# Kernel optimization log

Measured on AMD Instinct MI355X. Metric: run time of the kernel, lower is better.

The kernel has to match this reference:

```python
import jax, jax.numpy as jnp
import numpy as np


def setup_inputs() -> dict:
    key = jax.random.key(0)
    k1, k2, k3 = jax.random.split(key, 3)
    B, S, H, L = 64, 512, 768, 9  # batch, seq_len, bert hidden, num_labels
    sequence_output = jax.random.normal(k1, (B, S, H), dtype=jnp.float32)
    valid_mask = jax.random.randint(k2, (B, S), 0, 2, dtype=jnp.int32)
    W = jax.random.normal(k3, (H, L), dtype=jnp.float32) * 0.02  # TruncatedNormal stddev ~ initializer_range
    b = jnp.zeros((L,), dtype=jnp.float32)
    return {"sequence_output": sequence_output, "valid_mask": valid_mask, "W": W, "b": b}


def reference(sequence_output, valid_mask, W, b):
    # Per-row stream compaction: tokens with valid_mask==1 are moved to the
    # front of their row (stable order); remaining slots stay zero.
    B, S, H = sequence_output.shape
    pos = jnp.cumsum(valid_mask, axis=1) - 1           # destination index for valid tokens
    safe = jnp.where(valid_mask == 1, pos, S)           # invalid tokens -> dump slot S
    batch = jnp.arange(B)[:, None]                      # [B,1]
    valid_output = (
        jnp.zeros((B, S + 1, H), dtype=sequence_output.dtype)
        .at[batch, safe]
        .set(sequence_output)
    )[:, :S]                                            # drop dump slot
    # dropout is identity at inference (training=False)
    logits = jax.nn.softmax(valid_output @ W + b, axis=-1)  # [B,S,L]
    return logits
```

## Files before the change

### kernel.cpp

```cpp
#include <hip/hip_runtime.h>

#define B_ 64
#define S_ 512
#define H_ 768
#define L_ 9
#define TPB 16
#define BPR (S_ / TPB)
#define NPASS 1

__device__ __forceinline__ void bias_softmax(const float* __restrict__ bias,
                                             float* cprob) {
    float m = -3.4e38f;
#pragma unroll
    for (int c = 0; c < L_; c++) { cprob[c] = bias[c]; m = fmaxf(m, cprob[c]); }
    float s = 0.0f;
#pragma unroll
    for (int c = 0; c < L_; c++) { cprob[c] = __expf(cprob[c] - m); s += cprob[c]; }
    const float inv = 1.0f / s;
#pragma unroll
    for (int c = 0; c < L_; c++) cprob[c] *= inv;
}

__global__ __launch_bounds__(256, 4) void ner_kernel(const float* __restrict__ seq,
                                                     const int* __restrict__ mask,
                                                     const float* __restrict__ W,
                                                     const float* __restrict__ bias,
                                                     float* __restrict__ out) {
    __shared__ float wt[L_ * 3 * 64 * 4];
    __shared__ float bsh[16];
    __shared__ int   srcrow[S_];
    __shared__ int   wsum[4];

    const int tid  = threadIdx.x;
    const int lane = tid & 63;
    const int w    = tid >> 6;
    const int row  = blockIdx.x & 63;
    const int sub  = blockIdx.x >> 6;

    const int e0 = 2 * tid;
    const int2 mv = *reinterpret_cast<const int2*>(mask + row * S_ + e0);
    const int v0 = (mv.x != 0);
    const int v1 = (mv.y != 0);
    const unsigned long long b0 = __ballot(v0);
    const unsigned long long b1 = __ballot(v1);
    const unsigned long long lt = (1ULL << lane) - 1ULL;
    const int pfx  = __popcll(b0 & lt) + __popcll(b1 & lt);
    const int wtot = __popcll(b0) + __popcll(b1);
    if (lane == 0) wsum[w] = wtot;
    __syncthreads();

    const int cnt = wsum[0] + wsum[1] + wsum[2] + wsum[3];

    if (sub * TPB >= cnt) {
        float cprob[L_];
        bias_softmax(bias, cprob);
        const int base = (row * S_ + sub * TPB) * L_;
        for (int idx = tid; idx < TPB * L_; idx += 256)
            out[base + idx] = cprob[idx % L_];
        return;
    }

    int woff = 0;
#pragma unroll
    for (int i = 0; i < 4; i++)
        if (i < w) woff += wsum[i];
    const int p0 = woff + pfx;
    if (v0) srcrow[p0] = e0;
    if (v1) srcrow[p0 + v0] = e0 + 1;

    for (int idx = tid; idx < H_ * L_; idx += 256) {
        float val = W[idx];
        int h  = idx / 9;
        int c  = idx - 9 * h;
        int j  = h >> 8;
        int r  = h & 255;
        int ln = r >> 2;
        int k  = r & 3;
        wt[((c * 3 + j) * 64 + ln) * 4 + k] = val;
    }
    if (tid < 16) bsh[tid] = (tid < L_) ? bias[tid] : 0.0f;
    __syncthreads();

    const int cls = ((lane & 1) << 3) | (((lane >> 1) & 1) << 2)
                  | (((lane >> 2) & 1) << 1) | ((lane >> 3) & 1);
    const float bb = bsh[cls];
    const int g = lane >> 4;

    const float4* wt4 = reinterpret_cast<const float4*>(wt);

    for (int pass = 0; pass < NPASS; pass++) {
        const int basep = sub * TPB + w * (4 * NPASS) + pass * 4;

        if (basep >= cnt) {
            float cprob[L_];
            bias_softmax(bias, cprob);
            if (lane < 36)
                out[((size_t)row * S_ + basep) * L_ + lane] = cprob[lane % L_];
            continue;
        }

        float x[4][12];
#pragma unroll
        for (int t = 0; t < 4; t++) {
            const int pp = basep + t;
            if (pp < cnt) {
                const int src = srcrow[pp];
                const float4* p4 = reinterpret_cast<const float4*>(
                    seq + ((size_t)row * S_ + src) * H_) + lane;
                float4 a0 = p4[0], a1 = p4[64], a2 = p4[128];
                x[t][0] = a0.x; x[t][1] = a0.y; x[t][2]  = a0.z; x[t][3]  = a0.w;
                x[t][4] = a1.x; x[t][5] = a1.y; x[t][6]  = a1.z; x[t][7]  = a1.w;
                x[t][8] = a2.x; x[t][9] = a2.y; x[t][10] = a2.z; x[t][11] = a2.w;
            } else {
#pragma unroll
                for (int k = 0; k < 12; k++) x[t][k] = 0.0f;
            }
        }

        float acc[4][L_];
#pragma unroll
        for (int t = 0; t < 4; t++)
#pragma unroll
            for (int c = 0; c < L_; c++) acc[t][c] = 0.0f;

#pragma unroll
        for (int c = 0; c < L_; c++) {
#pragma unroll
            for (int j4 = 0; j4 < 3; j4++) {
                float4 wv = wt4[(c * 3 + j4) * 64 + lane];
#pragma unroll
                for (int t = 0; t < 4; t++) {
                    acc[t][c] += x[t][j4 * 4 + 0] * wv.x + x[t][j4 * 4 + 1] * wv.y
                               + x[t][j4 * 4 + 2] * wv.z + x[t][j4 * 4 + 3] * wv.w;
                }
            }
        }

        float logit[4];
#pragma unroll
        for (int t = 0; t < 4; t++) {
            float v[16];
#pragma unroll
            for (int c = 0; c < L_; c++) v[c] = acc[t][c];
#pragma unroll
            for (int c = L_; c < 16; c++) v[c] = 0.0f;

            {
                const bool b = (lane & 1);
#pragma unroll
                for (int i = 0; i < 8; i++) {
                    float give = b ? v[i] : v[i + 8];
                    float got  = __shfl_xor(give, 1);
                    v[i] = (b ? v[i + 8] : v[i]) + got;
                }
            }
            {
                const bool b = ((lane >> 1) & 1);
#pragma unroll
                for (int i = 0; i < 4; i++) {
                    float give = b ? v[i] : v[i + 4];
                    float got  = __shfl_xor(give, 2);
                    v[i] = (b ? v[i + 4] : v[i]) + got;
                }
            }
            {
                const bool b = ((lane >> 2) & 1);
#pragma unroll
                for (int i = 0; i < 2; i++) {
                    float give = b ? v[i] : v[i + 2];
                    float got  = __shfl_xor(give, 4);
                    v[i] = (b ? v[i + 2] : v[i]) + got;
                }
            }
            {
                const bool b = ((lane >> 3) & 1);
                float give = b ? v[0] : v[1];
                float got  = __shfl_xor(give, 8);
                v[0] = (b ? v[1] : v[0]) + got;
            }
            v[0] += __shfl_xor(v[0], 16);
            v[0] += __shfl_xor(v[0], 32);
            logit[t] = v[0];
        }

        float lg = (g == 0) ? logit[0] : (g == 1) ? logit[1]
                 : (g == 2) ? logit[2] : logit[3];
        lg += bb;
        float lx = (cls < L_) ? lg : -1e30f;
        float m = lx;
        m = fmaxf(m, __shfl_xor(m, 1));
        m = fmaxf(m, __shfl_xor(m, 2));
        m = fmaxf(m, __shfl_xor(m, 4));
        m = fmaxf(m, __shfl_xor(m, 8));
        float e = (cls < L_) ? __expf(lx - m) : 0.0f;
        float ssum = e;
        ssum += __shfl_xor(ssum, 1);
        ssum += __shfl_xor(ssum, 2);
        ssum += __shfl_xor(ssum, 4);
        ssum += __shfl_xor(ssum, 8);
        if (cls < L_)
            out[((size_t)row * S_ + basep + g) * L_ + cls] = e / ssum;
    }
}

extern "C" void kernel_launch(void* const* d_in, const int* in_sizes, int n_in,
                              void* d_out, int out_size, void* d_ws, size_t ws_size,
                              hipStream_t stream) {
    const float* seq  = (const float*)d_in[0];
    const int*   mask = (const int*)d_in[1];
    const float* W    = (const float*)d_in[2];
    const float* bias = (const float*)d_in[3];
    float*       out  = (float*)d_out;

    ner_kernel<<<B_ * BPR, 256, 0, stream>>>(seq, mask, W, bias, out);
}
```

Baseline: 147.0 us.

## Compute per-wave compaction via ballot select and issue token loads before weight staging

Each wave now reads the whole mask row itself and builds per-64-lane ballot prefix counts in registers, dropping the shared srcrow/wsum arrays and the first block barrier. Source rows are found with a binary popcount select, and the activation gathers are issued before the weight transpose into LDS so global latency overlaps the staging. The launch-bounds occupancy hint is removed and the bias is read from global memory. In exchange, every wave does redundant mask loads and select arithmetic, and register pressure rises because x is held across the barrier.

```diff
diff --git a/kernel.cpp b/kernel.cpp
--- a/kernel.cpp
+++ b/kernel.cpp
@@ -6,7 +6,6 @@
 #define L_ 9
 #define TPB 16
 #define BPR (S_ / TPB)
-#define NPASS 1
 
 __device__ __forceinline__ void bias_softmax(const float* __restrict__ bias,
                                              float* cprob) {
@@ -21,35 +20,33 @@
     for (int c = 0; c < L_; c++) cprob[c] *= inv;
 }
 
-__global__ __launch_bounds__(256, 4) void ner_kernel(const float* __restrict__ seq,
-                                                     const int* __restrict__ mask,
-                                                     const float* __restrict__ W,
-                                                     const float* __restrict__ bias,
-                                                     float* __restrict__ out) {
+__global__ __launch_bounds__(256) void ner_kernel(const float* __restrict__ seq,
+                                                  const int* __restrict__ mask,
+                                                  const float* __restrict__ W,
+                                                  const float* __restrict__ bias,
+                                                  float* __restrict__ out) {
     __shared__ float wt[L_ * 3 * 64 * 4];
-    __shared__ float bsh[16];
-    __shared__ int   srcrow[S_];
-    __shared__ int   wsum[4];
 
     const int tid  = threadIdx.x;
     const int lane = tid & 63;
-    const int w    = tid >> 6;
+    const int w    = __builtin_amdgcn_readfirstlane(tid >> 6);
     const int row  = blockIdx.x & 63;
     const int sub  = blockIdx.x >> 6;
 
-    const int e0 = 2 * tid;
-    const int2 mv = *reinterpret_cast<const int2*>(mask + row * S_ + e0);
-    const int v0 = (mv.x != 0);
-    const int v1 = (mv.y != 0);
-    const unsigned long long b0 = __ballot(v0);
-    const unsigned long long b1 = __ballot(v1);
-    const unsigned long long lt = (1ULL << lane) - 1ULL;
-    const int pfx  = __popcll(b0 & lt) + __popcll(b1 & lt);
-    const int wtot = __popcll(b0) + __popcll(b1);
-    if (lane == 0) wsum[w] = wtot;
-    __syncthreads();
-
-    const int cnt = wsum[0] + wsum[1] + wsum[2] + wsum[3];
+    const int* mrow = mask + row * S_;
+    int mv[8];
+#pragma unroll
+    for (int k = 0; k < 8; k++) mv[k] = mrow[64 * k + lane];
+
+    unsigned long long bm[8];
+    int csum[9];
+    csum[0] = 0;
+#pragma unroll
+    for (int k = 0; k < 8; k++) {
+        bm[k] = __ballot(mv[k] != 0);
+        csum[k + 1] = csum[k] + __popcll(bm[k]);
+    }
+    const int cnt = csum[8];
 
     if (sub * TPB >= cnt) {
         float cprob[L_];
@@ -60,13 +57,43 @@
         return;
     }
 
-    int woff = 0;
-#pragma unroll
-    for (int i = 0; i < 4; i++)
-        if (i < w) woff += wsum[i];
-    const int p0 = woff + pfx;
-    if (v0) srcrow[p0] = e0;
-    if (v1) srcrow[p0 + v0] = e0 + 1;
+    const int basep = sub * TPB + w * 4;
+
+    float x[4][12];
+#pragma unroll
+    for (int t = 0; t < 4; t++) {
+        const int pp = basep + t;
+        if (pp < cnt) {
+            int k = 0;
+#pragma unroll
+            for (int j = 1; j < 8; j++) k += (pp >= csum[j]);
+            int need = pp - csum[k];
+            unsigned long long xm = bm[k];
+            int src = 64 * k;
+            int c32 = __popcll(xm & 0xFFFFFFFFull);
+            if (need >= c32) { need -= c32; src += 32; xm >>= 32; }
+            int c16 = __popcll(xm & 0xFFFFull);
+            if (need >= c16) { need -= c16; src += 16; xm >>= 16; }
+            int c8  = __popcll(xm & 0xFFull);
+            if (need >= c8)  { need -= c8;  src += 8;  xm >>= 8; }
+            int c4  = __popcll(xm & 0xFull);
+            if (need >= c4)  { need -= c4;  src += 4;  xm >>= 4; }
+            int c2  = __popcll(xm & 0x3ull);
+            if (need >= c2)  { need -= c2;  src += 2;  xm >>= 2; }
+            int c1  = (int)(xm & 1ull);
+            if (need >= c1)  { src += 1; }
+
+            const float4* p4 = reinterpret_cast<const float4*>(
+                seq + ((size_t)row * S_ + src) * H_) + lane;
+            float4 a0 = p4[0], a1 = p4[64], a2 = p4[128];
+            x[t][0] = a0.x; x[t][1] = a0.y; x[t][2]  = a0.z; x[t][3]  = a0.w;
+            x[t][4] = a1.x; x[t][5] = a1.y; x[t][6]  = a1.z; x[t][7]  = a1.w;
+            x[t][8] = a2.x; x[t][9] = a2.y; x[t][10] = a2.z; x[t][11] = a2.w;
+        } else {
+#pragma unroll
+            for (int kk = 0; kk < 12; kk++) x[t][kk] = 0.0f;
+        }
+    }
 
     for (int idx = tid; idx < H_ * L_; idx += 256) {
         float val = W[idx];
@@ -78,129 +105,106 @@
         int k  = r & 3;
         wt[((c * 3 + j) * 64 + ln) * 4 + k] = val;
     }
-    if (tid < 16) bsh[tid] = (tid < L_) ? bias[tid] : 0.0f;
     __syncthreads();
 
     const int cls = ((lane & 1) << 3) | (((lane >> 1) & 1) << 2)
                   | (((lane >> 2) & 1) << 1) | ((lane >> 3) & 1);
-    const float bb = bsh[cls];
+    const float bb = (cls < L_) ? bias[cls] : 0.0f;
     const int g = lane >> 4;
 
+    if (basep >= cnt) {
+        float cprob[L_];
+        bias_softmax(bias, cprob);
+        if (lane < 36)
+            out[((size_t)row * S_ + basep) * L_ + lane] = cprob[lane % L_];
+        return;
+    }
+
     const float4* wt4 = reinterpret_cast<const float4*>(wt);
 
-    for (int pass = 0; pass < NPASS; pass++) {
-        const int basep = sub * TPB + w * (4 * NPASS) + pass * 4;
-
-        if (basep >= cnt) {
-            float cprob[L_];
-            bias_softmax(bias, cprob);
-            if (lane < 36)
-                out[((size_t)row * S_ + basep) * L_ + lane] = cprob[lane % L_];
-            continue;
-        }
-
-        float x[4][12];
-#pragma unroll
-        for (int t = 0; t < 4; t++) {
-            const int pp = basep + t;
-            if (pp < cnt) {
-                const int src = srcrow[pp];
-                const float4* p4 = reinterpret_cast<const float4*>(
-                    seq + ((size_t)row * S_ + src) * H_) + lane;
-                float4 a0 = p4[0], a1 = p4[64], a2 = p4[128];
-                x[t][0] = a0.x; x[t][1] = a0.y; x[t][2]  = a0.z; x[t][3]  = a0.w;
-                x[t][4] = a1.x; x[t][5] = a1.y; x[t][6]  = a1.z; x[t][7]  = a1.w;
-                x[t][8] = a2.x; x[t][9] = a2.y; x[t][10] = a2.z; x[t][11] = a2.w;
-            } else {
-#pragma unroll
-                for (int k = 0; k < 12; k++) x[t][k] = 0.0f;
-            }
-        }
-
-        float acc[4][L_];
-#pragma unroll
-        for (int t = 0; t < 4; t++)
-#pragma unroll
-            for (int c = 0; c < L_; c++) acc[t][c] = 0.0f;
-
-#pragma unroll
-        for (int c = 0; c < L_; c++) {
-#pragma unroll
-            for (int j4 = 0; j4 < 3; j4++) {
-                float4 wv = wt4[(c * 3 + j4) * 64 + lane];
-#pragma unroll
-                for (int t = 0; t < 4; t++) {
-                    acc[t][c] += x[t][j4 * 4 + 0] * wv.x + x[t][j4 * 4 + 1] * wv.y
-                               + x[t][j4 * 4 + 2] * wv.z + x[t][j4 * 4 + 3] * wv.w;
-                }
-            }
-        }
-
-        float logit[4];
-#pragma unroll
-        for (int t = 0; t < 4; t++) {
-            float v[16];
-#pragma unroll
-            for (int c = 0; c < L_; c++) v[c] = acc[t][c];
-#pragma unroll
-            for (int c = L_; c < 16; c++) v[c] = 0.0f;
-
-            {
-                const bool b = (lane & 1);
-#pragma unroll
-                for (int i = 0; i < 8; i++) {
-                    float give = b ? v[i] : v[i + 8];
-                    float got  = __shfl_xor(give, 1);
-                    v[i] = (b ? v[i + 8] : v[i]) + got;
-                }
-            }
-            {
-                const bool b = ((lane >> 1) & 1);
-#pragma unroll
-                for (int i = 0; i < 4; i++) {
-                    float give = b ? v[i] : v[i + 4];
-                    float got  = __shfl_xor(give, 2);
-                    v[i] = (b ? v[i + 4] : v[i]) + got;
-                }
-            }
-            {
-                const bool b = ((lane >> 2) & 1);
-#pragma unroll
-                for (int i = 0; i < 2; i++) {
-                    float give = b ? v[i] : v[i + 2];
-                    float got  = __shfl_xor(give, 4);
-                    v[i] = (b ? v[i + 2] : v[i]) + got;
-                }
-            }
-            {
-                const bool b = ((lane >> 3) & 1);
-                float give = b ? v[0] : v[1];
-                float got  = __shfl_xor(give, 8);
-                v[0] = (b ? v[1] : v[0]) + got;
-            }
-            v[0] += __shfl_xor(v[0], 16);
-            v[0] += __shfl_xor(v[0], 32);
-            logit[t] = v[0];
-        }
-
-        float lg = (g == 0) ? logit[0] : (g == 1) ? logit[1]
-                 : (g == 2) ? logit[2] : logit[3];
-        lg += bb;
-        float lx = (cls < L_) ? lg : -1e30f;
-        float m = lx;
-        m = fmaxf(m, __shfl_xor(m, 1));
-        m = fmaxf(m, __shfl_xor(m, 2));
-        m = fmaxf(m, __shfl_xor(m, 4));
-        m = fmaxf(m, __shfl_xor(m, 8));
-        float e = (cls < L_) ? __expf(lx - m) : 0.0f;
-        float ssum = e;
-        ssum += __shfl_xor(ssum, 1);
-        ssum += __shfl_xor(ssum, 2);
-        ssum += __shfl_xor(ssum, 4);
-        ssum += __shfl_xor(ssum, 8);
-        if (cls < L_)
-            out[((size_t)row * S_ + basep + g) * L_ + cls] = e / ssum;
-    }
+    float acc[4][L_];
+#pragma unroll
+    for (int t = 0; t < 4; t++)
+#pragma unroll
+        for (int c = 0; c < L_; c++) acc[t][c] = 0.0f;
+
+#pragma unroll
+    for (int c = 0; c < L_; c++) {
+#pragma unroll
+        for (int j4 = 0; j4 < 3; j4++) {
+            float4 wv = wt4[(c * 3 + j4) * 64 + lane];
+#pragma unroll
+            for (int t = 0; t < 4; t++) {
+                acc[t][c] += x[t][j4 * 4 + 0] * wv.x + x[t][j4 * 4 + 1] * wv.y
+                           + x[t][j4 * 4 + 2] * wv.z + x[t][j4 * 4 + 3] * wv.w;
+            }
+        }
+    }
+
+    float logit[4];
+#pragma unroll
+    for (int t = 0; t < 4; t++) {
+        float v[16];
+#pragma unroll
+        for (int c = 0; c < L_; c++) v[c] = acc[t][c];
+#pragma unroll
+        for (int c = L_; c < 16; c++) v[c] = 0.0f;
+
+        {
+            const bool b = (lane & 1);
+#pragma unroll
+            for (int i = 0; i < 8; i++) {
+                float give = b ? v[i] : v[i + 8];
+                float got  = __shfl_xor(give, 1);
+                v[i] = (b ? v[i + 8] : v[i]) + got;
+            }
+        }
+        {
+            const bool b = ((lane >> 1) & 1);
+#pragma unroll
+            for (int i = 0; i < 4; i++) {
+                float give = b ? v[i] : v[i + 4];
+                float got  = __shfl_xor(give, 2);
+                v[i] = (b ? v[i + 4] : v[i]) + got;
+            }
+        }
+        {
+            const bool b = ((lane >> 2) & 1);
+#pragma unroll
+            for (int i = 0; i < 2; i++) {
+                float give = b ? v[i] : v[i + 2];
+                float got  = __shfl_xor(give, 4);
+                v[i] = (b ? v[i + 2] : v[i]) + got;
+            }
+        }
+        {
+            const bool b = ((lane >> 3) & 1);
+            float give = b ? v[0] : v[1];
+            float got  = __shfl_xor(give, 8);
+            v[0] = (b ? v[1] : v[0]) + got;
+        }
+        v[0] += __shfl_xor(v[0], 16);
+        v[0] += __shfl_xor(v[0], 32);
+        logit[t] = v[0];
+    }
+
+    float lg = (g == 0) ? logit[0] : (g == 1) ? logit[1]
+             : (g == 2) ? logit[2] : logit[3];
+    lg += bb;
+    float lx = (cls < L_) ? lg : -1e30f;
+    float m = lx;
+    m = fmaxf(m, __shfl_xor(m, 1));
+    m = fmaxf(m, __shfl_xor(m, 2));
+    m = fmaxf(m, __shfl_xor(m, 4));
+    m = fmaxf(m, __shfl_xor(m, 8));
+    float e = (cls < L_) ? __expf(lx - m) : 0.0f;
+    float ssum = e;
+    ssum += __shfl_xor(ssum, 1);
+    ssum += __shfl_xor(ssum, 2);
+    ssum += __shfl_xor(ssum, 4);
+    ssum += __shfl_xor(ssum, 8);
+    if (cls < L_)
+        out[((size_t)row * S_ + basep + g) * L_ + cls] = e / ssum;
 }
 
 extern "C" void kernel_launch(void* const* d_in, const int* in_sizes, int n_in,
```

After: 150.6 us. +2.4%, slower.
